# Kernel optimization log

Hardware: AMD Instinct MI355X
Metric: run time of the kernel (lower is better)

Reference implementation:

```python
import jax, jax.numpy as jnp
import numpy as np

N = 50000; E = 800000
IN = 128; H = 4; D = 32; OH = H * D; AIN = 2 * IN
SCALE = float(1.0 / np.sqrt(IN))

def _ln(x, g, b):
    m = jnp.mean(x, -1, keepdims=True)
    v = jnp.mean((x - m) ** 2, -1, keepdims=True)
    return (x - m) * jax.lax.rsqrt(v + 1e-5) * g + b

def setup_inputs():
    keys = iter(jax.random.split(jax.random.key(0), 24))
    nrm = lambda shape, s=1.0: jax.random.normal(next(keys), shape, dtype=jnp.float32) * s
    inp = {}
    inp['x0'] = nrm((N, IN)); inp['x1'] = nrm((N, IN)); inp['x99'] = nrm((N, AIN))
    inp['feat0'] = jax.random.uniform(next(keys), (E, 2), dtype=jnp.float32)
    inp['feat1'] = jax.random.uniform(next(keys), (E, 2), dtype=jnp.float32)
    for nm, shape in [('Wq', (IN, OH)), ('Wk', (IN, OH)), ('Wv', (IN, OH)), ('Wo', (OH, OH)), ('Wffn', (IN, OH)), ('Waq', (AIN, OH)), ('Wak', (AIN, OH)), ('Wav', (AIN, OH)), ('Wao', (OH, OH)), ('Waffn', (AIN, OH))]:
        inp[nm] = nrm(shape, 0.05)
    for nm in ['bq', 'bk', 'bv', 'bo', 'bffn', 'baq', 'bak', 'bav', 'bao', 'baffn', 'ln_b', 'aln_b']:
        inp[nm] = jnp.zeros((OH,), jnp.float32)
    inp['ln_g'] = jnp.ones((OH,), jnp.float32); inp['aln_g'] = jnp.ones((OH,), jnp.float32)
    for nm in ['src0', 'dst0', 'src1', 'dst1']:
        inp[nm] = jax.random.randint(next(keys), (E,), 0, N, dtype=jnp.int32)
    return inp

def _forward(x0, x1, x99, feat0, feat1, Wq, bq, Wk, bk, Wv, bv, Wo, bo, Wffn, bffn, ln_g, ln_b, Waq, baq, Wak, bak, Wav, bav, Wao, bao, Waffn, baffn, aln_g, aln_b, src0, dst0, src1, dst1):
    proj = lambda x, W, b: (x @ W + b).reshape(x.shape[0], H, D)
    xs = (x0, x1)
    edges = ((src0, dst0, feat0), (src1, dst1, feat1))
    q = [proj(x, Wq, bq) for x in xs]   # per-v_id linears are shared
    k = [proj(x, Wk, bk) for x in xs]
    v = [proj(x, Wv, bv) for x in xs]
    q99 = proj(x99, Waq, baq); k99 = proj(x99, Wak, bak); v99 = proj(x99, Wav, bav)
    aggr_outs = []
    for i, (src, dst, feat) in enumerate(edges):  # loop over the 2 edge types (structural)
        f = feat[:, None, 0:1]  # [E,1,1] 'connect' edge weight
        s = jnp.sum(k[i][src] * q[i][dst], -1, keepdims=True) * f   # [E,H,1]
        s99 = jnp.sum(k99[src] * q99[dst], -1, keepdims=True) * f
        s = jnp.exp(jnp.clip(s * SCALE, -5.0, 5.0))
        s99 = jnp.exp(jnp.clip(s99 * SCALE, -5.0, 5.0))
        wv = jax.ops.segment_sum(v[i][src] * s, dst, num_segments=N)    # [N,H,D]
        z = jax.ops.segment_sum(s, dst, num_segments=N)                 # [N,H,1]
        wv99 = jax.ops.segment_sum(v99[src] * s99, dst, num_segments=N)
        z99 = jax.ops.segment_sum(s99, dst, num_segments=N)
        # per-v_id branch (h_dict in original; computed but not returned by the module)
        o = (wv / (z + 1.0)).reshape(N, OH) @ Wo + bo
        h = xs[i] @ Wffn + bffn + o
        h = h + _ln(h, ln_g, ln_b)
        # aggregated (node 99) branch -> returned as aggr_h_dict[v_id]
        ao = (wv99 / (z99 + 1.0)).reshape(N, OH) @ Wao + bao
        ah = x99 @ Waffn + baffn + ao
        ah = ah + _ln(ah, aln_g, aln_b)
        aggr_outs.append(ah)
    return tuple(aggr_outs)

def reference(x0, x1, x99, feat0, feat1, Wq, bq, Wk, bk, Wv, bv, Wo, bo, Wffn, bffn, ln_g, ln_b, Waq, baq, Wak, bak, Wav, bav, Wao, bao, Waffn, baffn, aln_g, aln_b, src0, dst0, src1, dst1):
    return _forward(x0, x1, x99, feat0, feat1, Wq, bq, Wk, bk, Wv, bv, Wo, bo, Wffn, bffn, ln_g, ln_b, Waq, baq, Wak, bak, Wav, bav, Wao, bao, Waffn, baffn, aln_g, aln_b, src0, dst0, src1, dst1)
```

## Files before the change

kernel.cpp:

```cpp
#include <hip/hip_runtime.h>
#include <math.h>

#define NN 50000
#define EE 800000
#define AIN 256
#define OH 128

#define NTOT  (2 * NN)
#define NB    391
#define CAP   5120

typedef __attribute__((ext_vector_type(8))) short bf16x8;
typedef __attribute__((ext_vector_type(4))) float f32x4;
typedef __attribute__((ext_vector_type(2))) float f32x2;

static __device__ __forceinline__ unsigned short f2bf(float f) {
    union { float f; unsigned int u; } v; v.f = f;
    return (unsigned short)((v.u + 0x7FFFu + ((v.u >> 16) & 1u)) >> 16);
}
static __device__ __forceinline__ float bflo(unsigned int u) { return __uint_as_float(u << 16); }
static __device__ __forceinline__ float bfhi(unsigned int u) { return __uint_as_float(u & 0xFFFF0000u); }

__global__ __launch_bounds__(256) void cvt_x_k(const float* __restrict__ x, unsigned short* __restrict__ xb)
{
    const int i = blockIdx.x * 256 + threadIdx.x;
    if (i >= NN * AIN / 4) return;
    const float4 v = ((const float4*)x)[i];
    ushort4 o;
    o.x = f2bf(v.x); o.y = f2bf(v.y); o.z = f2bf(v.z); o.w = f2bf(v.w);
    ((ushort4*)xb)[i] = o;
}

__global__ __launch_bounds__(256) void cvt_w_k(
    const float* __restrict__ Wq, const float* __restrict__ Wk,
    const float* __restrict__ Wv, const float* __restrict__ Wf,
    const float* __restrict__ Wo, unsigned short* __restrict__ Wt,
    unsigned short* __restrict__ Waot)
{
    const int n = blockIdx.x;
    const int k = threadIdx.x;
    if (n < 512) {
        const float* W = (n < 128) ? Wq : (n < 256) ? Wk : (n < 384) ? Wv : Wf;
        Wt[(size_t)n * 256 + k] = f2bf(W[(size_t)k * OH + (n & 127)]);
    } else {
        if (k < 128) Waot[(size_t)(n - 512) * 128 + k] = f2bf(Wo[(size_t)k * OH + (n - 512)]);
    }
}

__global__ __launch_bounds__(256) void qkvf_mfma_k(
    const unsigned short* __restrict__ xb,
    const unsigned short* __restrict__ Wt,
    const float* __restrict__ bq, const float* __restrict__ bk,
    const float* __restrict__ bv, const float* __restrict__ bf,
    unsigned short* __restrict__ qb, unsigned char* __restrict__ kv8,
    unsigned short* __restrict__ ffnb, int M)
{
    __shared__ unsigned short As[128][40];
    __shared__ unsigned short Bs[128][40];
    const int tid  = threadIdx.x;
    const int lane = tid & 63;
    const int wave = tid >> 6;
    const int wr = wave >> 1, wc = wave & 1;
    const int quad = lane >> 4, m16 = lane & 15;
    const int row0 = blockIdx.x * 128;
    const int col0 = blockIdx.y * 128;

    f32x4 acc[4][4];
    #pragma unroll
    for (int i = 0; i < 4; ++i)
        #pragma unroll
        for (int j = 0; j < 4; ++j) acc[i][j] = 0.f;

    const int lr  = tid >> 1;
    const int lkh = (tid & 1) * 16;

    for (int kt = 0; kt < 256; kt += 32) {
        uint4 a0 = {0,0,0,0}, a1 = {0,0,0,0};
        const int grow = row0 + lr;
        if (grow < M) {
            const uint4* p = (const uint4*)(xb + (size_t)grow * 256 + kt + lkh);
            a0 = p[0]; a1 = p[1];
        }
        *(uint4*)&As[lr][lkh]     = a0;
        *(uint4*)&As[lr][lkh + 8] = a1;
        const uint4* wp = (const uint4*)(Wt + (size_t)(col0 + lr) * 256 + kt + lkh);
        *(uint4*)&Bs[lr][lkh]     = wp[0];
        *(uint4*)&Bs[lr][lkh + 8] = wp[1];
        __syncthreads();
        bf16x8 af[4], bfr[4];
        #pragma unroll
        for (int t = 0; t < 4; ++t) af[t]  = *(const bf16x8*)&As[wr * 64 + t * 16 + m16][quad * 8];
        #pragma unroll
        for (int t = 0; t < 4; ++t) bfr[t] = *(const bf16x8*)&Bs[wc * 64 + t * 16 + m16][quad * 8];
        #pragma unroll
        for (int i = 0; i < 4; ++i)
            #pragma unroll
            for (int j = 0; j < 4; ++j)
                acc[i][j] = __builtin_amdgcn_mfma_f32_16x16x32_bf16(af[i], bfr[j], acc[i][j], 0, 0, 0);
        __syncthreads();
    }

    const int y = blockIdx.y;
    const float* bias = (y == 0) ? bq : (y == 1) ? bk : (y == 2) ? bv : bf;

    if (y == 1 || y == 2) {
        const int ocol = (y == 2) ? 128 : 0;
        #pragma unroll
        for (int i = 0; i < 4; ++i)
            #pragma unroll
            for (int j = 0; j < 4; ++j) {
                const int col = wc * 64 + j * 16 + m16;
                const float b = bias[col];
                #pragma unroll
                for (int r = 0; r < 4; ++r) {
                    const int row = row0 + wr * 64 + i * 16 + quad * 4 + r;
                    if (row < M) {
                        const unsigned int pk =
                            (unsigned int)__builtin_amdgcn_cvt_pk_fp8_f32(acc[i][j][r] + b, 0.f, 0, 0);
                        kv8[(size_t)row * 256 + ocol + col] = (unsigned char)(pk & 0xFF);
                    }
                }
            }
    } else {
        unsigned short* obase = (y == 3) ? ffnb : qb;
        #pragma unroll
        for (int i = 0; i < 4; ++i)
            #pragma unroll
            for (int j = 0; j < 4; ++j) {
                const int col = wc * 64 + j * 16 + m16;
                const float b = bias[col];
                #pragma unroll
                for (int r = 0; r < 4; ++r) {
                    const int row = row0 + wr * 64 + i * 16 + quad * 4 + r;
                    if (row < M) obase[(size_t)row * 128 + col] = f2bf(acc[i][j][r] + b);
                }
            }
    }
}

__global__ __launch_bounds__(256) void binpass_k(
    const int* __restrict__ dst0, const int* __restrict__ dst1,
    const int* __restrict__ src0, const int* __restrict__ src1,
    const float* __restrict__ feat0, const float* __restrict__ feat1,
    int* __restrict__ cursor, uint2* __restrict__ stage)
{
    __shared__ int hcnt[NB], blkbase[NB], lcur[NB];
    const int tid = threadIdx.x;
    const long base = (long)blockIdx.x * 8192;

    for (int i = tid; i < NB; i += 256) { hcnt[i] = 0; lcur[i] = 0; }
    __syncthreads();

    for (int i = tid; i < 8192; i += 256) {
        const long e = base + i;
        if (e < 2L * EE) {
            const int nid = (e < EE) ? dst0[e] : NN + dst1[e - EE];
            atomicAdd(&hcnt[nid >> 8], 1);
        }
    }
    __syncthreads();
    for (int i = tid; i < NB; i += 256)
        if (hcnt[i]) blkbase[i] = atomicAdd(&cursor[i], hcnt[i]);
    __syncthreads();

    for (int i = tid; i < 8192; i += 256) {
        const long e = base + i;
        if (e < 2L * EE) {
            const bool a = (e < EE);
            const int ee = a ? (int)e : (int)(e - EE);
            const int nid = a ? dst0[ee] : NN + dst1[ee];
            const int s = a ? src0[ee] : src1[ee];
            const float f = a ? feat0[(size_t)ee * 2] : feat1[(size_t)ee * 2];
            const int bk = nid >> 8;
            const int r = atomicAdd(&lcur[bk], 1);
            uint2 rec;
            rec.x = __float_as_uint(f);
            rec.y = ((unsigned int)s << 8) | (unsigned int)(nid & 255);
            stage[(size_t)bk * CAP + blkbase[bk] + r] = rec;
        }
    }
}

__global__ __launch_bounds__(512) void bscan_k(const int* __restrict__ cursor, int* __restrict__ bbase)
{
    __shared__ int part[512];
    const int t = threadIdx.x;
    const int v = (t < NB) ? cursor[t] : 0;
    part[t] = v;
    __syncthreads();
    for (int st = 1; st < 512; st <<= 1) {
        int u = (t >= st) ? part[t - st] : 0;
        __syncthreads();
        part[t] += u;
        __syncthreads();
    }
    if (t < NB) bbase[t] = part[t] - v;
}

__global__ __launch_bounds__(256) void sortpass_k(
    const uint2* __restrict__ stage, const int* __restrict__ cursor,
    const int* __restrict__ bbase, uint2* __restrict__ erec,
    int* __restrict__ off, int* __restrict__ deg)
{
    __shared__ int h[256], eb[256], cur[256];
    const int b = blockIdx.x;
    const int t = threadIdx.x;
    const int cntb = cursor[b];
    const int obase = bbase[b];
    const uint2* sb = stage + (size_t)b * CAP;

    h[t] = 0; cur[t] = 0;
    __syncthreads();
    for (int i = t; i < cntb; i += 256) atomicAdd(&h[(int)(sb[i].y & 255u)], 1);
    __syncthreads();
    eb[t] = h[t];
    __syncthreads();
    for (int st = 1; st < 256; st <<= 1) {
        int u = (t >= st) ? eb[t - st] : 0;
        __syncthreads();
        eb[t] += u;
        __syncthreads();
    }
    const int incl = eb[t];
    __syncthreads();
    eb[t] = incl - h[t];
    __syncthreads();

    const int nid = b * 256 + t;
    if (nid < NTOT) {
        off[nid] = obase + eb[t];
        deg[nid] = h[t];
    }

    for (int i = t; i < cntb; i += 256) {
        const uint2 r = sb[i];
        const int loc = (int)(r.y & 255u);
        const int rk = atomicAdd(&cur[loc], 1);
        uint2 o;
        o.x = r.y >> 8;
        o.y = r.x;
        erec[obase + eb[loc] + rk] = o;
    }
}

__global__ __launch_bounds__(256) void aggregate_k(
    const unsigned short* __restrict__ qb, const unsigned char* __restrict__ kv8,
    const uint2* __restrict__ erec,
    const int* __restrict__ off, const int* __restrict__ deg,
    unsigned short* __restrict__ att)
{
    const int nid = blockIdx.x * 4 + (threadIdx.x >> 6);
    if (nid >= NTOT) return;
    const int n = (nid >= NN) ? nid - NN : nid;
    const int lane = threadIdx.x & 63;
    const int g   = lane >> 4;
    const int d16 = lane & 15;
    const int start = off[nid];
    const int count = deg[nid];

    const uint4 qu = *(const uint4*)(qb + (size_t)n * 128 + d16 * 8);
    f32x2 qd0, qd1, qd2, qd3;
    qd0[0] = bflo(qu.x); qd0[1] = bfhi(qu.x);
    qd1[0] = bflo(qu.y); qd1[1] = bfhi(qu.y);
    qd2[0] = bflo(qu.z); qd2[1] = bfhi(qu.z);
    qd3[0] = bflo(qu.w); qd3[1] = bfhi(qu.w);

    f32x2 av0 = 0.f, av1 = 0.f, av2 = 0.f, av3 = 0.f;
    float zp = 0.f;
    const float SCALE = 0.088388347648318447f;
    const unsigned char* kvl = kv8 + d16 * 8;

    for (int base = 0; base < count; base += 64) {
        const int m = min(64, count - base);
        const uint2 rr = erec[start + base + min(lane, m - 1)];
        int src = __shfl((int)rr.x, g);
        const unsigned char* rp = kvl + (size_t)src * 256;
        uint2 kc = *(const uint2*)rp;
        uint2 vc = *(const uint2*)(rp + 128);
        for (int j0 = 0; j0 < m; j0 += 4) {
            const uint2 kk = kc;
            const uint2 vv = vc;
            const float f = __int_as_float(__shfl((int)rr.y, j0 + g));
            const int jn = j0 + 4;
            if (jn < m) {
                src = __shfl((int)rr.x, jn + g);
                const unsigned char* rn = kvl + (size_t)src * 256;
                kc = *(const uint2*)rn;
                vc = *(const uint2*)(rn + 128);
            }
            const f32x2 k0 = __builtin_amdgcn_cvt_pk_f32_fp8((int)kk.x, false);
            const f32x2 k1 = __builtin_amdgcn_cvt_pk_f32_fp8((int)kk.x, true);
            const f32x2 k2 = __builtin_amdgcn_cvt_pk_f32_fp8((int)kk.y, false);
            const f32x2 k3 = __builtin_amdgcn_cvt_pk_f32_fp8((int)kk.y, true);
            f32x2 p2 = k0 * qd0;
            p2 += k1 * qd1;
            p2 += k2 * qd2;
            p2 += k3 * qd3;
            float p = p2[0] + p2[1];
            p += __shfl_xor(p, 1);
            p += __shfl_xor(p, 2);
            float sc = __expf(fminf(5.f, fmaxf(-5.f, p * f * SCALE)));
            sc = (j0 + g < m) ? sc : 0.f;
            zp += sc;
            const f32x2 v0 = __builtin_amdgcn_cvt_pk_f32_fp8((int)vv.x, false);
            const f32x2 v1 = __builtin_amdgcn_cvt_pk_f32_fp8((int)vv.x, true);
            const f32x2 v2 = __builtin_amdgcn_cvt_pk_f32_fp8((int)vv.y, false);
            const f32x2 v3 = __builtin_amdgcn_cvt_pk_f32_fp8((int)vv.y, true);
            f32x2 sc2; sc2[0] = sc; sc2[1] = sc;
            av0 += v0 * sc2;
            av1 += v1 * sc2;
            av2 += v2 * sc2;
            av3 += v3 * sc2;
        }
    }

    float z = zp;
    z += __shfl_xor(z, 16);
    z += __shfl_xor(z, 32);
    av0[0] += __shfl_xor(av0[0], 16); av0[0] += __shfl_xor(av0[0], 32);
    av0[1] += __shfl_xor(av0[1], 16); av0[1] += __shfl_xor(av0[1], 32);
    av1[0] += __shfl_xor(av1[0], 16); av1[0] += __shfl_xor(av1[0], 32);
    av1[1] += __shfl_xor(av1[1], 16); av1[1] += __shfl_xor(av1[1], 32);
    av2[0] += __shfl_xor(av2[0], 16); av2[0] += __shfl_xor(av2[0], 32);
    av2[1] += __shfl_xor(av2[1], 16); av2[1] += __shfl_xor(av2[1], 32);
    av3[0] += __shfl_xor(av3[0], 16); av3[0] += __shfl_xor(av3[0], 32);
    av3[1] += __shfl_xor(av3[1], 16); av3[1] += __shfl_xor(av3[1], 32);

    const float inv = 1.f / (z + 1.f);
    const f32x2 e01 = (g & 1) ? av1 : av0;
    const f32x2 e23 = (g & 1) ? av3 : av2;
    const f32x2 e   = (g & 2) ? e23 : e01;
    const float ax = e[0] * inv;
    const float ay = e[1] * inv;
    const unsigned int o = ((unsigned int)f2bf(ay) << 16) | (unsigned int)f2bf(ax);
    *(unsigned int*)(att + (size_t)nid * 128 + d16 * 8 + g * 2) = o;
}

__global__ __launch_bounds__(256) void attn_out_mfma_k(
    const unsigned short* __restrict__ attAll, const unsigned short* __restrict__ Wt,
    const float* __restrict__ bo, const unsigned short* __restrict__ ffnb,
    const float* __restrict__ g, const float* __restrict__ bln,
    float* __restrict__ Yall, int M)
{
    __shared__ unsigned short As[128][40];
    __shared__ unsigned short Bs[128][40];
    __shared__ float rsum[2][128], rsq[2][128];
    __shared__ float meanar[128], invar[128];

    const unsigned short* att = attAll + (size_t)blockIdx.y * NN * 128;
    float* Y = Yall + (size_t)blockIdx.y * NN * 128;

    const int tid  = threadIdx.x;
    const int lane = tid & 63;
    const int wave = tid >> 6;
    const int wr = wave >> 1, wc = wave & 1;
    const int quad = lane >> 4, m16 = lane & 15;
    const int row0 = blockIdx.x * 128;

    f32x4 acc[4][4];
    #pragma unroll
    for (int i = 0; i < 4; ++i)
        #pragma unroll
        for (int j = 0; j < 4; ++j) acc[i][j] = 0.f;

    const int lr  = tid >> 1;
    const int lkh = (tid & 1) * 16;

    for (int kt = 0; kt < 128; kt += 32) {
        uint4 a0 = {0,0,0,0}, a1 = {0,0,0,0};
        const int grow = row0 + lr;
        if (grow < M) {
            const uint4* p = (const uint4*)(att + (size_t)grow * 128 + kt + lkh);
            a0 = p[0]; a1 = p[1];
        }
        *(uint4*)&As[lr][lkh]     = a0;
        *(uint4*)&As[lr][lkh + 8] = a1;
        const uint4* wp = (const uint4*)(Wt + (size_t)lr * 128 + kt + lkh);
        *(uint4*)&Bs[lr][lkh]     = wp[0];
        *(uint4*)&Bs[lr][lkh + 8] = wp[1];
        __syncthreads();
        bf16x8 af[4], bfr[4];
        #pragma unroll
        for (int t = 0; t < 4; ++t) af[t]  = *(const bf16x8*)&As[wr * 64 + t * 16 + m16][quad * 8];
        #pragma unroll
        for (int t = 0; t < 4; ++t) bfr[t] = *(const bf16x8*)&Bs[wc * 64 + t * 16 + m16][quad * 8];
        #pragma unroll
        for (int i = 0; i < 4; ++i)
            #pragma unroll
            for (int j = 0; j < 4; ++j)
                acc[i][j] = __builtin_amdgcn_mfma_f32_16x16x32_bf16(af[i], bfr[j], acc[i][j], 0, 0, 0);
        __syncthreads();
    }

    #pragma unroll
    for (int i = 0; i < 4; ++i) {
        #pragma unroll
        for (int r = 0; r < 4; ++r) {
            const int rl = wr * 64 + i * 16 + quad * 4 + r;
            const int grow = row0 + rl;
            float s = 0.f, q = 0.f;
            #pragma unroll
            for (int j = 0; j < 4; ++j) {
                const int col = wc * 64 + j * 16 + m16;
                float v = acc[i][j][r] + bo[col];
                if (grow < M) v += bflo(ffnb[(size_t)grow * 128 + col]);
                acc[i][j][r] = v;
                s += v; q += v * v;
            }
            #pragma unroll
            for (int mm = 1; mm <= 8; mm <<= 1) {
                s += __shfl_xor(s, mm, 16);
                q += __shfl_xor(q, mm, 16);
            }
            if (m16 == 0) { rsum[wc][rl] = s; rsq[wc][rl] = q; }
        }
    }
    __syncthreads();
    if (tid < 128) {
        const float s = rsum[0][tid] + rsum[1][tid];
        const float q = rsq[0][tid] + rsq[1][tid];
        const float mean = s * (1.f / 128.f);
        const float var  = q * (1.f / 128.f) - mean * mean;
        meanar[tid] = mean;
        invar[tid]  = rsqrtf(fmaxf(var, 0.f) + 1e-5f);
    }
    __syncthreads();

    #pragma unroll
    for (int i = 0; i < 4; ++i) {
        #pragma unroll
        for (int j = 0; j < 4; ++j) {
            const int col = wc * 64 + j * 16 + m16;
            const float gv = g[col], lv = bln[col];
            #pragma unroll
            for (int r = 0; r < 4; ++r) {
                const int rl = wr * 64 + i * 16 + quad * 4 + r;
                const int grow = row0 + rl;
                if (grow < M) {
                    const float v = acc[i][j][r];
                    Y[(size_t)grow * 128 + col] = v + (v - meanar[rl]) * invar[rl] * gv + lv;
                }
            }
        }
    }
}

extern "C" void kernel_launch(void* const* d_in, const int* in_sizes, int n_in,
                              void* d_out, int out_size, void* d_ws, size_t ws_size,
                              hipStream_t stream) {
    const float* x99   = (const float*)d_in[2];
    const float* feat0 = (const float*)d_in[3];
    const float* feat1 = (const float*)d_in[4];
    const float* Waq   = (const float*)d_in[10];
    const float* Wak   = (const float*)d_in[11];
    const float* Wav   = (const float*)d_in[12];
    const float* Wao   = (const float*)d_in[13];
    const float* Waffn = (const float*)d_in[14];
    const float* baq   = (const float*)d_in[20];
    const float* bak   = (const float*)d_in[21];
    const float* bav   = (const float*)d_in[22];
    const float* bao   = (const float*)d_in[23];
    const float* baffn = (const float*)d_in[24];
    const float* aln_b = (const float*)d_in[26];
    const float* aln_g = (const float*)d_in[28];
    const int* src0 = (const int*)d_in[29];
    const int* dst0 = (const int*)d_in[30];
    const int* src1 = (const int*)d_in[31];
    const int* dst1 = (const int*)d_in[32];

    unsigned short* xb   = (unsigned short*)d_ws;
    unsigned short* qb   = xb + (size_t)NN * 256;
    unsigned char*  kv8  = (unsigned char*)(qb + (size_t)NN * 128);
    unsigned short* ffnb = (unsigned short*)(kv8 + (size_t)NN * 256);
    unsigned short* att  = ffnb + (size_t)NN * 128;
    unsigned short* Wt   = att  + (size_t)NTOT * 128;
    unsigned short* Waot = Wt   + (size_t)512 * 256;
    int* cursor = (int*)(Waot + 128 * 128);
    int* bbase  = cursor + NB;
    int* off    = bbase + NB;
    int* deg    = off + NTOT;

    float* out = (float*)d_out;
    uint2* stage = (uint2*)d_out;
    uint2* erec  = stage + (size_t)NB * CAP;

    cvt_x_k<<<(NN * AIN / 4 + 255) / 256, 256, 0, stream>>>(x99, xb);
    cvt_w_k<<<640, 256, 0, stream>>>(Waq, Wak, Wav, Waffn, Wao, Wt, Waot);

    const int mtiles = (NN + 127) / 128;
    qkvf_mfma_k<<<dim3(mtiles, 4), 256, 0, stream>>>(xb, Wt, baq, bak, bav, baffn, qb, kv8, ffnb, NN);

    hipMemsetAsync(cursor, 0, NB * sizeof(int), stream);
    binpass_k<<<(2 * EE + 8191) / 8192, 256, 0, stream>>>(
        dst0, dst1, src0, src1, feat0, feat1, cursor, stage);
    bscan_k<<<1, 512, 0, stream>>>(cursor, bbase);
    sortpass_k<<<NB, 256, 0, stream>>>(stage, cursor, bbase, erec, off, deg);

    aggregate_k<<<(NTOT + 3) / 4, 256, 0, stream>>>(qb, kv8, erec, off, deg, att);
    attn_out_mfma_k<<<dim3(mtiles, 2), 256, 0, stream>>>(att, Waot, bao, ffnb, aln_g, aln_b, out, NN);
}
```

Measured before the change: 432.8 us.

## Pack edge records to 32 bits, stage sort in LDS, XCD-aware GEMM block mapping

Edge records shrink from 8 bytes to one 32-bit word: the source index sits in the high 17 bits and the edge weight is quantized to 15 bits. This halves the erec traffic in the sort and aggregate kernels. The sort pass now loads each bin's staged records into LDS once instead of reading global memory twice. Both GEMM kernels use a 1D grid remapped so that consecutive row tiles and their column/set siblings land on the same XCD, aiming for better L2 reuse. The cost is a 40KB LDS footprint that can lower occupancy, plus precision loss from quantizing the edge weight.

```diff
diff --git a/kernel.cpp b/kernel.cpp
--- a/kernel.cpp
+++ b/kernel.cpp
@@ -9,6 +9,8 @@
 #define NTOT  (2 * NN)
 #define NB    391
 #define CAP   5120
+#define MT    391
+#define RPX   49
 
 typedef __attribute__((ext_vector_type(8))) short bf16x8;
 typedef __attribute__((ext_vector_type(4))) float f32x4;
@@ -55,6 +57,13 @@
     unsigned short* __restrict__ qb, unsigned char* __restrict__ kv8,
     unsigned short* __restrict__ ffnb, int M)
 {
+    const int nblk = blockIdx.x;
+    const int xcd  = nblk & 7;
+    const int slot = nblk >> 3;
+    const int rowt = xcd * RPX + (slot >> 2);
+    const int y    = slot & 3;
+    if (rowt >= MT) return;
+
     __shared__ unsigned short As[128][40];
     __shared__ unsigned short Bs[128][40];
     const int tid  = threadIdx.x;
@@ -62,8 +71,8 @@
     const int wave = tid >> 6;
     const int wr = wave >> 1, wc = wave & 1;
     const int quad = lane >> 4, m16 = lane & 15;
-    const int row0 = blockIdx.x * 128;
-    const int col0 = blockIdx.y * 128;
+    const int row0 = rowt * 128;
+    const int col0 = y * 128;
 
     f32x4 acc[4][4];
     #pragma unroll
@@ -100,7 +109,6 @@
         __syncthreads();
     }
 
-    const int y = blockIdx.y;
     const float* bias = (y == 0) ? bq : (y == 1) ? bk : (y == 2) ? bv : bf;
 
     if (y == 1 || y == 2) {
@@ -199,19 +207,21 @@
 
 __global__ __launch_bounds__(256) void sortpass_k(
     const uint2* __restrict__ stage, const int* __restrict__ cursor,
-    const int* __restrict__ bbase, uint2* __restrict__ erec,
+    const int* __restrict__ bbase, unsigned int* __restrict__ erec,
     int* __restrict__ off, int* __restrict__ deg)
 {
+    __shared__ uint2 srec[CAP];
     __shared__ int h[256], eb[256], cur[256];
     const int b = blockIdx.x;
     const int t = threadIdx.x;
-    const int cntb = cursor[b];
+    const int cntb = min(cursor[b], CAP);
     const int obase = bbase[b];
     const uint2* sb = stage + (size_t)b * CAP;
 
     h[t] = 0; cur[t] = 0;
-    __syncthreads();
-    for (int i = t; i < cntb; i += 256) atomicAdd(&h[(int)(sb[i].y & 255u)], 1);
+    for (int i = t; i < cntb; i += 256) srec[i] = sb[i];
+    __syncthreads();
+    for (int i = t; i < cntb; i += 256) atomicAdd(&h[(int)(srec[i].y & 255u)], 1);
     __syncthreads();
     eb[t] = h[t];
     __syncthreads();
@@ -233,19 +243,17 @@
     }
 
     for (int i = t; i < cntb; i += 256) {
-        const uint2 r = sb[i];
+        const uint2 r = srec[i];
         const int loc = (int)(r.y & 255u);
         const int rk = atomicAdd(&cur[loc], 1);
-        uint2 o;
-        o.x = r.y >> 8;
-        o.y = r.x;
-        erec[obase + eb[loc] + rk] = o;
+        const unsigned int f15 = __float2uint_rn(__uint_as_float(r.x) * 32767.f);
+        erec[obase + eb[loc] + rk] = ((r.y >> 8) << 15) | f15;
     }
 }
 
 __global__ __launch_bounds__(256) void aggregate_k(
     const unsigned short* __restrict__ qb, const unsigned char* __restrict__ kv8,
-    const uint2* __restrict__ erec,
+    const unsigned int* __restrict__ erec,
     const int* __restrict__ off, const int* __restrict__ deg,
     unsigned short* __restrict__ att)
 {
@@ -268,23 +276,24 @@
     f32x2 av0 = 0.f, av1 = 0.f, av2 = 0.f, av3 = 0.f;
     float zp = 0.f;
     const float SCALE = 0.088388347648318447f;
+    const float FDEQ  = 1.0f / 32767.0f;
     const unsigned char* kvl = kv8 + d16 * 8;
 
     for (int base = 0; base < count; base += 64) {
         const int m = min(64, count - base);
-        const uint2 rr = erec[start + base + min(lane, m - 1)];
-        int src = __shfl((int)rr.x, g);
-        const unsigned char* rp = kvl + (size_t)src * 256;
+        const unsigned int ue = erec[start + base + min(lane, m - 1)];
+        unsigned int cu = (unsigned int)__shfl((int)ue, g);
+        const unsigned char* rp = kvl + (size_t)(cu >> 15) * 256;
         uint2 kc = *(const uint2*)rp;
         uint2 vc = *(const uint2*)(rp + 128);
         for (int j0 = 0; j0 < m; j0 += 4) {
             const uint2 kk = kc;
             const uint2 vv = vc;
-            const float f = __int_as_float(__shfl((int)rr.y, j0 + g));
+            const float f = (float)(cu & 32767u) * FDEQ;
             const int jn = j0 + 4;
             if (jn < m) {
-                src = __shfl((int)rr.x, jn + g);
-                const unsigned char* rn = kvl + (size_t)src * 256;
+                cu = (unsigned int)__shfl((int)ue, jn + g);
+                const unsigned char* rn = kvl + (size_t)(cu >> 15) * 256;
                 kc = *(const uint2*)rn;
                 vc = *(const uint2*)(rn + 128);
             }
@@ -342,20 +351,27 @@
     const float* __restrict__ g, const float* __restrict__ bln,
     float* __restrict__ Yall, int M)
 {
+    const int nblk = blockIdx.x;
+    const int xcd  = nblk & 7;
+    const int slot = nblk >> 3;
+    const int rowt = xcd * RPX + (slot >> 1);
+    const int set  = slot & 1;
+    if (rowt >= MT) return;
+
     __shared__ unsigned short As[128][40];
     __shared__ unsigned short Bs[128][40];
     __shared__ float rsum[2][128], rsq[2][128];
     __shared__ float meanar[128], invar[128];
 
-    const unsigned short* att = attAll + (size_t)blockIdx.y * NN * 128;
-    float* Y = Yall + (size_t)blockIdx.y * NN * 128;
+    const unsigned short* att = attAll + (size_t)set * NN * 128;
+    float* Y = Yall + (size_t)set * NN * 128;
 
     const int tid  = threadIdx.x;
     const int lane = tid & 63;
     const int wave = tid >> 6;
     const int wr = wave >> 1, wc = wave & 1;
     const int quad = lane >> 4, m16 = lane & 15;
-    const int row0 = blockIdx.x * 128;
+    const int row0 = rowt * 128;
 
     f32x4 acc[4][4];
     #pragma unroll
@@ -482,13 +498,12 @@
 
     float* out = (float*)d_out;
     uint2* stage = (uint2*)d_out;
-    uint2* erec  = stage + (size_t)NB * CAP;
+    unsigned int* erec = (unsigned int*)(stage + (size_t)NB * CAP);
 
     cvt_x_k<<<(NN * AIN / 4 + 255) / 256, 256, 0, stream>>>(x99, xb);
     cvt_w_k<<<640, 256, 0, stream>>>(Waq, Wak, Wav, Waffn, Wao, Wt, Waot);
 
-    const int mtiles = (NN + 127) / 128;
-    qkvf_mfma_k<<<dim3(mtiles, 4), 256, 0, stream>>>(xb, Wt, baq, bak, bav, baffn, qb, kv8, ffnb, NN);
+    qkvf_mfma_k<<<8 * RPX * 4, 256, 0, stream>>>(xb, Wt, baq, bak, bav, baffn, qb, kv8, ffnb, NN);
 
     hipMemsetAsync(cursor, 0, NB * sizeof(int), stream);
     binpass_k<<<(2 * EE + 8191) / 8192, 256, 0, stream>>>(
@@ -497,5 +512,5 @@
     sortpass_k<<<NB, 256, 0, stream>>>(stage, cursor, bbase, erec, off, deg);
 
     aggregate_k<<<(NTOT + 3) / 4, 256, 0, stream>>>(qb, kv8, erec, off, deg, att);
-    attn_out_mfma_k<<<dim3(mtiles, 2), 256, 0, stream>>>(att, Waot, bao, ffnb, aln_g, aln_b, out, NN);
-}
+    attn_out_mfma_k<<<8 * RPX * 2, 256, 0, stream>>>(att, Waot, bao, ffnb, aln_g, aln_b, out, NN);
+}
```

New measurement: 431.8 us. Within noise of the previous version (-0.2%).
